# Optimization experiments

Hardware: AMD Instinct MI355X
Metric: run time of the kernel (lower is better)

The kernel has to match this reference:

```python
import jax, jax.numpy as jnp
import numpy as np

D_MODEL = 768
H = 12
D_K = D_MODEL // H
B = 2
S = 2048
NEG = -1e9


def setup_inputs() -> dict:
    key = jax.random.key(0)
    ks = jax.random.split(key, 12)
    scale = 1.0 / np.sqrt(D_MODEL)
    inp = {
        "q": jax.random.normal(ks[0], (B, S, D_MODEL), jnp.float32),
        "k": jax.random.normal(ks[1], (B, S, D_MODEL), jnp.float32),
        "v": jax.random.normal(ks[2], (B, S, D_MODEL), jnp.float32),
        "mask": jax.random.randint(ks[3], (B, 1, S, S), 0, 2, jnp.int32),
        "Wq": jax.random.normal(ks[4], (D_MODEL, D_MODEL), jnp.float32) * scale,
        "bq": jnp.zeros((D_MODEL,), jnp.float32),
        "Wk": jax.random.normal(ks[5], (D_MODEL, D_MODEL), jnp.float32) * scale,
        "bk": jnp.zeros((D_MODEL,), jnp.float32),
        "Wv": jax.random.normal(ks[6], (D_MODEL, D_MODEL), jnp.float32) * scale,
        "bv": jnp.zeros((D_MODEL,), jnp.float32),
        "Wo": jax.random.normal(ks[7], (D_MODEL, D_MODEL), jnp.float32) * scale,
        "bo": jnp.zeros((D_MODEL,), jnp.float32),
    }
    return inp


def _split_heads(x):
    # [B, S, D] -> [B, H, S, D_K]
    b, s, _ = x.shape
    return x.reshape(b, s, H, D_K).transpose(0, 2, 1, 3)


def reference(q, k, v, mask, Wq, bq, Wk, bk, Wv, bv, Wo, bo):
    # torch Linear: x @ W.T + b
    query = _split_heads(q @ Wq.T + bq)
    key_ = _split_heads(k @ Wk.T + bk)
    value = _split_heads(v @ Wv.T + bv)

    scores = jnp.einsum("bhqd,bhkd->bhqk", query, key_) / np.sqrt(D_K)
    scores = jnp.where(mask == 0, NEG, scores)
    attn = jax.nn.softmax(scores, axis=-1)  # dropout p=0.0 -> identity

    x = jnp.einsum("bhqk,bhkd->bhqd", attn, value)
    x = x.transpose(0, 2, 1, 3).reshape(q.shape[0], -1, D_MODEL)
    return x @ Wo.T + bo
```

## Files before the change

### kernel.cpp

```cpp
#include <hip/hip_runtime.h>
#include <math.h>

#define DMODEL 768
#define NHEAD 12
#define DKDIM 64
#define BB 2
#define SS 2048
#define MROWS (BB * SS)
#define WELEM (DMODEL * DMODEL)

typedef unsigned short bf16_t;
typedef __attribute__((ext_vector_type(8))) short s8;
typedef __attribute__((ext_vector_type(4))) float f4;

#define MFMA(a, b, c) __builtin_amdgcn_mfma_f32_16x16x32_bf16((a), (b), (c), 0, 0, 0)

__device__ __forceinline__ bf16_t f2bf(float f) {
    unsigned u = __float_as_uint(f);
    u += 0x7fffu + ((u >> 16) & 1u);
    return (bf16_t)(u >> 16);
}
__device__ __forceinline__ unsigned pack2(float a, float b) {
    return (unsigned)f2bf(a) | ((unsigned)f2bf(b) << 16);
}
__device__ __forceinline__ s8 ldfrag(const bf16_t* p) {
    union { uint4 u; s8 s; } x;
    x.u = *(const uint4*)p;
    return x.s;
}

__device__ __forceinline__ void ld_stage(const bf16_t* p, uint4& u0, uint4& u1) {
    u0 = *(const uint4*)p;
    u1 = *(const uint4*)(p + 8);
}
__device__ __forceinline__ void ld_stage(const float* p, uint4& u0, uint4& u1) {
    const float4 f0 = *(const float4*)p;
    const float4 f1 = *(const float4*)(p + 4);
    const float4 f2 = *(const float4*)(p + 8);
    const float4 f3 = *(const float4*)(p + 12);
    u0.x = pack2(f0.x, f0.y); u0.y = pack2(f0.z, f0.w);
    u0.z = pack2(f1.x, f1.y); u0.w = pack2(f1.z, f1.w);
    u1.x = pack2(f2.x, f2.y); u1.y = pack2(f2.z, f2.w);
    u1.z = pack2(f3.x, f3.y); u1.w = pack2(f3.z, f3.w);
}

__global__ void cvt_weights(const float* __restrict__ W0, const float* __restrict__ W1,
                            const float* __restrict__ W2, const float* __restrict__ W3,
                            bf16_t* __restrict__ dst)
{
    const float* src = (blockIdx.y == 0) ? W0 : (blockIdx.y == 1) ? W1
                     : (blockIdx.y == 2) ? W2 : W3;
    bf16_t* d = dst + (size_t)blockIdx.y * WELEM;
    const int i = (blockIdx.x * 256 + threadIdx.x) * 4;
    const float4 v = *(const float4*)(src + i);
    ushort4 h;
    h.x = f2bf(v.x); h.y = f2bf(v.y); h.z = f2bf(v.z); h.w = f2bf(v.w);
    *(ushort4*)(d + i) = h;
}

template<typename TA, typename TO>
__global__ __launch_bounds__(256) void gemm_tiled(
    const TA* __restrict__ A0, const TA* __restrict__ A1, const TA* __restrict__ A2,
    const bf16_t* __restrict__ W0, const bf16_t* __restrict__ W1, const bf16_t* __restrict__ W2,
    const float* __restrict__ bias0, const float* __restrict__ bias1, const float* __restrict__ bias2,
    TO* __restrict__ C0, TO* __restrict__ C1, TO* __restrict__ C2)
{
    __shared__ uint4 As4[128 * 4];
    __shared__ uint4 Bs4[128 * 4];

    const int z = blockIdx.z;
    const TA*     A    = (z == 0) ? A0 : (z == 1) ? A1 : A2;
    const bf16_t* W    = (z == 0) ? W0 : (z == 1) ? W1 : W2;
    const float*  bias = (z == 0) ? bias0 : (z == 1) ? bias1 : bias2;
    TO*           C    = (z == 0) ? C0 : (z == 1) ? C1 : C2;

    const int tid  = threadIdx.x;
    const int lane = tid & 63;
    const int w    = tid >> 6;
    const int wm   = w & 1;
    const int wn   = w >> 1;
    const int l15  = lane & 15;
    const int quad = lane >> 4;
    const int m0   = blockIdx.y * 128;
    const int n0   = blockIdx.x * 128;

    const int srow  = tid >> 1;
    const int shalf = tid & 1;
    const int sw    = srow & 3;

    const TA*     aptr = A + (size_t)(m0 + srow) * DMODEL + shalf * 16;
    const bf16_t* wptr = W + (size_t)(n0 + srow) * DMODEL + shalf * 16;

    f4 acc[4][4];
    #pragma unroll
    for (int i = 0; i < 4; i++)
        #pragma unroll
        for (int j = 0; j < 4; j++)
            acc[i][j] = (f4){0.f, 0.f, 0.f, 0.f};

    for (int k0 = 0; k0 < DMODEL; k0 += 32) {
        uint4 au0, au1, bu0, bu1;
        ld_stage(aptr + k0, au0, au1);
        ld_stage(wptr + k0, bu0, bu1);
        __syncthreads();
        As4[srow * 4 + ((shalf * 2 + 0) ^ sw)] = au0;
        As4[srow * 4 + ((shalf * 2 + 1) ^ sw)] = au1;
        Bs4[srow * 4 + ((shalf * 2 + 0) ^ sw)] = bu0;
        Bs4[srow * 4 + ((shalf * 2 + 1) ^ sw)] = bu1;
        __syncthreads();

        s8 af[4], bf[4];
        #pragma unroll
        for (int t = 0; t < 4; t++) {
            const int ar = wm * 64 + t * 16 + l15;
            const int br = wn * 64 + t * 16 + l15;
            union { uint4 u; s8 s; } xa, xb;
            xa.u = As4[ar * 4 + (quad ^ (ar & 3))];
            xb.u = Bs4[br * 4 + (quad ^ (br & 3))];
            af[t] = xa.s;
            bf[t] = xb.s;
        }
        #pragma unroll
        for (int mt = 0; mt < 4; mt++)
            #pragma unroll
            for (int nt = 0; nt < 4; nt++)
                acc[mt][nt] = MFMA(af[mt], bf[nt], acc[mt][nt]);
    }

    #pragma unroll
    for (int mt = 0; mt < 4; mt++) {
        #pragma unroll
        for (int nt = 0; nt < 4; nt++) {
            const int col = n0 + wn * 64 + nt * 16 + l15;
            const float bb = bias[col];
            #pragma unroll
            for (int reg = 0; reg < 4; reg++) {
                const int row = m0 + wm * 64 + mt * 16 + quad * 4 + reg;
                const float val = acc[mt][nt][reg] + bb;
                TO* dst = C + (size_t)row * DMODEL + col;
                if constexpr (sizeof(TO) == 2) *dst = f2bf(val);
                else                           *dst = val;
            }
        }
    }
}

__global__ __launch_bounds__(256) void attn_mfma(
    const bf16_t* __restrict__ Q, const bf16_t* __restrict__ K,
    const bf16_t* __restrict__ V, const int* __restrict__ mask,
    bf16_t* __restrict__ O)
{
    __shared__ unsigned Vs[64][36];
    __shared__ unsigned Ps[4][16][36];

    const int tid  = threadIdx.x;
    const int lane = tid & 63;
    const int w    = tid >> 6;
    const int l15  = lane & 15;
    const int quad = lane >> 4;
    const int q0   = blockIdx.x * 64;
    const int h    = blockIdx.y;
    const int b    = blockIdx.z;
    const size_t base = ((size_t)b * SS) * DMODEL + (size_t)h * DKDIM;

    const bf16_t* qrow = Q + base + (size_t)(q0 + w * 16 + l15) * DMODEL + quad * 8;
    const s8 qf0 = ldfrag(qrow);
    const s8 qf1 = ldfrag(qrow + 32);

    f4 oacc[4];
    float m_run[4], l_run[4];
    #pragma unroll
    for (int i = 0; i < 4; i++) {
        oacc[i] = (f4){0.f, 0.f, 0.f, 0.f};
        m_run[i] = -3.0e30f; l_run[i] = 0.0f;
    }

    const int kp  = tid & 31;
    const int oct = tid >> 5;

    const int* mrow = mask + (size_t)b * SS * SS + (size_t)(q0 + w * 16 + quad * 4) * SS;

    for (int k0 = 0; k0 < SS; k0 += 64) {
        const bf16_t* vrow = V + base + (size_t)(k0 + 2 * kp) * DMODEL + oct * 8;
        const uint4 va = *(const uint4*)vrow;
        const uint4 vb = *(const uint4*)(vrow + DMODEL);
        __syncthreads();
        {
            const unsigned short* pa = (const unsigned short*)&va;
            const unsigned short* pb = (const unsigned short*)&vb;
            #pragma unroll
            for (int i = 0; i < 8; i++)
                Vs[oct * 8 + i][kp] = (unsigned)pa[i] | ((unsigned)pb[i] << 16);
        }

        f4 sacc[4];
        #pragma unroll
        for (int nt = 0; nt < 4; nt++) {
            const bf16_t* krow = K + base + (size_t)(k0 + nt * 16 + l15) * DMODEL + quad * 8;
            f4 zz = {0.f, 0.f, 0.f, 0.f};
            zz = MFMA(qf0, ldfrag(krow), zz);
            zz = MFMA(qf1, ldfrag(krow + 32), zz);
            sacc[nt] = zz;
        }

        float p[4][4];
        #pragma unroll
        for (int reg = 0; reg < 4; reg++) {
            float sv[4];
            #pragma unroll
            for (int nt = 0; nt < 4; nt++) {
                const int mk = mrow[(size_t)reg * SS + k0 + nt * 16 + l15];
                sv[nt] = mk ? sacc[nt][reg] * 0.125f : -1.0e9f;
            }
            float mx = fmaxf(fmaxf(sv[0], sv[1]), fmaxf(sv[2], sv[3]));
            mx = fmaxf(mx, __shfl_xor(mx, 1, 16));
            mx = fmaxf(mx, __shfl_xor(mx, 2, 16));
            mx = fmaxf(mx, __shfl_xor(mx, 4, 16));
            mx = fmaxf(mx, __shfl_xor(mx, 8, 16));

            const float m_new = fmaxf(m_run[reg], mx);
            const float alpha = __expf(m_run[reg] - m_new);
            float rs = 0.f;
            #pragma unroll
            for (int nt = 0; nt < 4; nt++) {
                p[reg][nt] = __expf(sv[nt] - m_new);
                rs += p[reg][nt];
            }
            rs += __shfl_xor(rs, 1, 16);
            rs += __shfl_xor(rs, 2, 16);
            rs += __shfl_xor(rs, 4, 16);
            rs += __shfl_xor(rs, 8, 16);

            l_run[reg] = l_run[reg] * alpha + rs;
            m_run[reg] = m_new;
            #pragma unroll
            for (int dt = 0; dt < 4; dt++) oacc[dt][reg] *= alpha;
        }

        #pragma unroll
        for (int reg = 0; reg < 4; reg++) {
            #pragma unroll
            for (int nt = 0; nt < 4; nt++) {
                const float mine  = p[reg][nt];
                const float other = __shfl_xor(mine, 1, 16);
                if ((lane & 1) == 0)
                    Ps[w][quad * 4 + reg][nt * 8 + (l15 >> 1)] = pack2(mine, other);
            }
        }
        __syncthreads();

        #pragma unroll
        for (int kt = 0; kt < 2; kt++) {
            union { uint4 u; s8 s; } pf;
            pf.u = *(const uint4*)&Ps[w][l15][kt * 16 + quad * 4];
            #pragma unroll
            for (int dt = 0; dt < 4; dt++) {
                union { uint4 u; s8 s; } vf;
                vf.u = *(const uint4*)&Vs[dt * 16 + l15][kt * 16 + quad * 4];
                oacc[dt] = MFMA(pf.s, vf.s, oacc[dt]);
            }
        }
    }

    #pragma unroll
    for (int reg = 0; reg < 4; reg++) {
        const float inv = 1.0f / l_run[reg];
        #pragma unroll
        for (int dt = 0; dt < 4; dt++) {
            O[base + (size_t)(q0 + w * 16 + quad * 4 + reg) * DMODEL + dt * 16 + l15] =
                f2bf(oacc[dt][reg] * inv);
        }
    }
}

extern "C" void kernel_launch(void* const* d_in, const int* in_sizes, int n_in,
                              void* d_out, int out_size, void* d_ws, size_t ws_size,
                              hipStream_t stream)
{
    const float* q    = (const float*)d_in[0];
    const float* k    = (const float*)d_in[1];
    const float* v    = (const float*)d_in[2];
    const int*   mask = (const int*)  d_in[3];
    const float* Wq   = (const float*)d_in[4];
    const float* bq   = (const float*)d_in[5];
    const float* Wk   = (const float*)d_in[6];
    const float* bk   = (const float*)d_in[7];
    const float* Wv   = (const float*)d_in[8];
    const float* bv   = (const float*)d_in[9];
    const float* Wo   = (const float*)d_in[10];
    const float* bo   = (const float*)d_in[11];
    float* out = (float*)d_out;

    bf16_t* wsb = (bf16_t*)d_ws;
    const size_t plane = (size_t)MROWS * DMODEL;
    bf16_t* Qp  = wsb;
    bf16_t* Kp  = wsb + plane;
    bf16_t* Vp  = wsb + 2 * plane;
    bf16_t* Ctx = wsb + 3 * plane;
    bf16_t* Wqb = wsb + 4 * plane;
    bf16_t* Wkb = Wqb + WELEM;
    bf16_t* Wvb = Wkb + WELEM;
    bf16_t* Wob = Wvb + WELEM;

    cvt_weights<<<dim3(WELEM / 1024, 4), 256, 0, stream>>>(Wq, Wk, Wv, Wo, Wqb);

    gemm_tiled<float, bf16_t><<<dim3(DMODEL / 128, MROWS / 128, 3), 256, 0, stream>>>(
        q, k, v, Wqb, Wkb, Wvb, bq, bk, bv, Qp, Kp, Vp);

    attn_mfma<<<dim3(SS / 64, NHEAD, BB), 256, 0, stream>>>(Qp, Kp, Vp, mask, Ctx);

    gemm_tiled<bf16_t, float><<<dim3(DMODEL / 128, MROWS / 128, 1), 256, 0, stream>>>(
        Ctx, Ctx, Ctx, Wob, Wob, Wob, bo, bo, bo, out, out, out);
}
```

Measured before the change: 342.9 us.

## Bit-pack mask, split attention over keys, prefetch V, fold softmax scale into Q

Adds a pre-pass that packs the int32 mask into 64-bit ballot words, so the attention kernel reads one word per row per key tile instead of many int loads that are re-read for every head. The attention kernel is split into two key halves to double the grid, with a separate combine kernel that merges the partial outputs using the saved max and sum. V loads are register-prefetched one tile ahead, and the 1/sqrt(dk) scale is moved into the Q projection epilogue. The split adds fp32 partial-output traffic and an extra launch, and the mask pre-pass still reads the full 32 MB mask once.

```diff
diff --git a/kernel.cpp b/kernel.cpp
--- a/kernel.cpp
+++ b/kernel.cpp
@@ -8,6 +8,10 @@
 #define SS 2048
 #define MROWS (BB * SS)
 #define WELEM (DMODEL * DMODEL)
+#define NSPLIT 2
+#define KCHUNK (SS / NSPLIT)
+#define AROWS (BB * NHEAD * SS)
+#define MWORDS (SS / 64)
 
 typedef unsigned short bf16_t;
 typedef __attribute__((ext_vector_type(8))) short s8;
@@ -58,12 +62,22 @@
     *(ushort4*)(d + i) = h;
 }
 
+__global__ __launch_bounds__(256) void mask_to_bits(
+    const int* __restrict__ mask, unsigned long long* __restrict__ mbits)
+{
+    const size_t gid = (size_t)blockIdx.x * 256 + threadIdx.x;
+    const int m = mask[gid];
+    const unsigned long long bal = __ballot(m != 0);
+    if ((threadIdx.x & 63) == 0) mbits[gid >> 6] = bal;
+}
+
 template<typename TA, typename TO>
 __global__ __launch_bounds__(256) void gemm_tiled(
     const TA* __restrict__ A0, const TA* __restrict__ A1, const TA* __restrict__ A2,
     const bf16_t* __restrict__ W0, const bf16_t* __restrict__ W1, const bf16_t* __restrict__ W2,
     const float* __restrict__ bias0, const float* __restrict__ bias1, const float* __restrict__ bias2,
-    TO* __restrict__ C0, TO* __restrict__ C1, TO* __restrict__ C2)
+    TO* __restrict__ C0, TO* __restrict__ C1, TO* __restrict__ C2,
+    float sc0, float sc1, float sc2)
 {
     __shared__ uint4 As4[128 * 4];
     __shared__ uint4 Bs4[128 * 4];
@@ -73,6 +87,7 @@
     const bf16_t* W    = (z == 0) ? W0 : (z == 1) ? W1 : W2;
     const float*  bias = (z == 0) ? bias0 : (z == 1) ? bias1 : bias2;
     TO*           C    = (z == 0) ? C0 : (z == 1) ? C1 : C2;
+    const float   sc   = (z == 0) ? sc0 : (z == 1) ? sc1 : sc2;
 
     const int tid  = threadIdx.x;
     const int lane = tid & 63;
@@ -136,7 +151,7 @@
             #pragma unroll
             for (int reg = 0; reg < 4; reg++) {
                 const int row = m0 + wm * 64 + mt * 16 + quad * 4 + reg;
-                const float val = acc[mt][nt][reg] + bb;
+                const float val = (acc[mt][nt][reg] + bb) * sc;
                 TO* dst = C + (size_t)row * DMODEL + col;
                 if constexpr (sizeof(TO) == 2) *dst = f2bf(val);
                 else                           *dst = val;
@@ -145,10 +160,10 @@
     }
 }
 
-__global__ __launch_bounds__(256) void attn_mfma(
+__global__ __launch_bounds__(256, 6) void attn_mfma(
     const bf16_t* __restrict__ Q, const bf16_t* __restrict__ K,
-    const bf16_t* __restrict__ V, const int* __restrict__ mask,
-    bf16_t* __restrict__ O)
+    const bf16_t* __restrict__ V, const unsigned long long* __restrict__ mbits,
+    float* __restrict__ Opart, float2* __restrict__ Ml)
 {
     __shared__ unsigned Vs[64][36];
     __shared__ unsigned Ps[4][16][36];
@@ -160,7 +175,10 @@
     const int quad = lane >> 4;
     const int q0   = blockIdx.x * 64;
     const int h    = blockIdx.y;
-    const int b    = blockIdx.z;
+    const int zz   = blockIdx.z;
+    const int b     = zz >> 1;
+    const int split = zz & 1;
+    const int ks    = split * KCHUNK;
     const size_t base = ((size_t)b * SS) * DMODEL + (size_t)h * DKDIM;
 
     const bf16_t* qrow = Q + base + (size_t)(q0 + w * 16 + l15) * DMODEL + quad * 8;
@@ -177,13 +195,15 @@
 
     const int kp  = tid & 31;
     const int oct = tid >> 5;
-
-    const int* mrow = mask + (size_t)b * SS * SS + (size_t)(q0 + w * 16 + quad * 4) * SS;
-
-    for (int k0 = 0; k0 < SS; k0 += 64) {
-        const bf16_t* vrow = V + base + (size_t)(k0 + 2 * kp) * DMODEL + oct * 8;
-        const uint4 va = *(const uint4*)vrow;
-        const uint4 vb = *(const uint4*)(vrow + DMODEL);
+    const bf16_t* vbase = V + base + (size_t)(2 * kp) * DMODEL + oct * 8;
+
+    const unsigned long long* mbase =
+        mbits + ((size_t)b * SS + (q0 + w * 16 + quad * 4)) * MWORDS;
+
+    uint4 va = *(const uint4*)(vbase + (size_t)ks * DMODEL);
+    uint4 vb = *(const uint4*)(vbase + (size_t)ks * DMODEL + DMODEL);
+
+    for (int k0 = ks; k0 < ks + KCHUNK; k0 += 64) {
         __syncthreads();
         {
             const unsigned short* pa = (const unsigned short*)&va;
@@ -192,26 +212,36 @@
             for (int i = 0; i < 8; i++)
                 Vs[oct * 8 + i][kp] = (unsigned)pa[i] | ((unsigned)pb[i] << 16);
         }
+        if (k0 + 64 < ks + KCHUNK) {
+            va = *(const uint4*)(vbase + (size_t)(k0 + 64) * DMODEL);
+            vb = *(const uint4*)(vbase + (size_t)(k0 + 64) * DMODEL + DMODEL);
+        }
+        unsigned long long mw[4];
+        #pragma unroll
+        for (int reg = 0; reg < 4; reg++)
+            mw[reg] = mbase[(size_t)reg * MWORDS + (k0 >> 6)];
 
         f4 sacc[4];
         #pragma unroll
         for (int nt = 0; nt < 4; nt++) {
             const bf16_t* krow = K + base + (size_t)(k0 + nt * 16 + l15) * DMODEL + quad * 8;
-            f4 zz = {0.f, 0.f, 0.f, 0.f};
-            zz = MFMA(qf0, ldfrag(krow), zz);
-            zz = MFMA(qf1, ldfrag(krow + 32), zz);
-            sacc[nt] = zz;
+            f4 zz2 = {0.f, 0.f, 0.f, 0.f};
+            zz2 = MFMA(qf0, ldfrag(krow), zz2);
+            zz2 = MFMA(qf1, ldfrag(krow + 32), zz2);
+            sacc[nt] = zz2;
         }
 
         float p[4][4];
         #pragma unroll
         for (int reg = 0; reg < 4; reg++) {
+            const unsigned mlo = ((unsigned)mw[reg]) >> l15;
+            const unsigned mhi = ((unsigned)(mw[reg] >> 32)) >> l15;
             float sv[4];
-            #pragma unroll
-            for (int nt = 0; nt < 4; nt++) {
-                const int mk = mrow[(size_t)reg * SS + k0 + nt * 16 + l15];
-                sv[nt] = mk ? sacc[nt][reg] * 0.125f : -1.0e9f;
-            }
+            sv[0] = (mlo & 1u)       ? sacc[0][reg] : -1.0e9f;
+            sv[1] = (mlo & 0x10000u) ? sacc[1][reg] : -1.0e9f;
+            sv[2] = (mhi & 1u)       ? sacc[2][reg] : -1.0e9f;
+            sv[3] = (mhi & 0x10000u) ? sacc[3][reg] : -1.0e9f;
+
             float mx = fmaxf(fmaxf(sv[0], sv[1]), fmaxf(sv[2], sv[3]));
             mx = fmaxf(mx, __shfl_xor(mx, 1, 16));
             mx = fmaxf(mx, __shfl_xor(mx, 2, 16));
@@ -262,15 +292,51 @@
         }
     }
 
+    const int rid0 = (b * NHEAD + h) * SS + q0 + w * 16 + quad * 4;
     #pragma unroll
     for (int reg = 0; reg < 4; reg++) {
-        const float inv = 1.0f / l_run[reg];
-        #pragma unroll
-        for (int dt = 0; dt < 4; dt++) {
-            O[base + (size_t)(q0 + w * 16 + quad * 4 + reg) * DMODEL + dt * 16 + l15] =
-                f2bf(oacc[dt][reg] * inv);
-        }
-    }
+        float* dst = Opart + ((size_t)split * AROWS + rid0 + reg) * DKDIM;
+        #pragma unroll
+        for (int dt = 0; dt < 4; dt++)
+            dst[dt * 16 + l15] = oacc[dt][reg];
+        if (l15 == 0)
+            Ml[(size_t)split * AROWS + rid0 + reg] = make_float2(m_run[reg], l_run[reg]);
+    }
+}
+
+__global__ __launch_bounds__(256) void attn_combine(
+    const float* __restrict__ Opart, const float2* __restrict__ Ml,
+    bf16_t* __restrict__ Ctx)
+{
+    const int gid   = blockIdx.x * 256 + threadIdx.x;
+    const int rid   = gid >> 2;
+    const int dpart = (gid & 3) * 16;
+
+    const float2 ml0 = Ml[rid];
+    const float2 ml1 = Ml[AROWS + rid];
+    const float m   = fmaxf(ml0.x, ml1.x);
+    const float w0  = __expf(ml0.x - m);
+    const float w1  = __expf(ml1.x - m);
+    const float inv = 1.0f / (ml0.y * w0 + ml1.y * w1);
+
+    const float* o0 = Opart + (size_t)rid * DKDIM + dpart;
+    const float* o1 = o0 + (size_t)AROWS * DKDIM;
+
+    const int q  = rid & (SS - 1);
+    const int bh = rid >> 11;
+    const int hh = bh % NHEAD;
+    const int bb = bh / NHEAD;
+    bf16_t* dst = Ctx + ((size_t)bb * SS + q) * DMODEL + hh * DKDIM + dpart;
+
+    unsigned out[8];
+    #pragma unroll
+    for (int i = 0; i < 8; i++) {
+        const float a = (o0[2 * i]     * w0 + o1[2 * i]     * w1) * inv;
+        const float c = (o0[2 * i + 1] * w0 + o1[2 * i + 1] * w1) * inv;
+        out[i] = pack2(a, c);
+    }
+    *(uint4*)dst       = *(const uint4*)&out[0];
+    *(uint4*)(dst + 8) = *(const uint4*)&out[4];
 }
 
 extern "C" void kernel_launch(void* const* d_in, const int* in_sizes, int n_in,
@@ -301,14 +367,21 @@
     bf16_t* Wkb = Wqb + WELEM;
     bf16_t* Wvb = Wkb + WELEM;
     bf16_t* Wob = Wvb + WELEM;
+    float*  Opart = (float*)(Wob + WELEM);
+    float2* Ml    = (float2*)(Opart + (size_t)NSPLIT * AROWS * DKDIM);
+    unsigned long long* mbits = (unsigned long long*)(Ml + (size_t)NSPLIT * AROWS);
 
     cvt_weights<<<dim3(WELEM / 1024, 4), 256, 0, stream>>>(Wq, Wk, Wv, Wo, Wqb);
+    mask_to_bits<<<dim3((BB * SS * SS) / 256), 256, 0, stream>>>(mask, mbits);
 
     gemm_tiled<float, bf16_t><<<dim3(DMODEL / 128, MROWS / 128, 3), 256, 0, stream>>>(
-        q, k, v, Wqb, Wkb, Wvb, bq, bk, bv, Qp, Kp, Vp);
-
-    attn_mfma<<<dim3(SS / 64, NHEAD, BB), 256, 0, stream>>>(Qp, Kp, Vp, mask, Ctx);
+        q, k, v, Wqb, Wkb, Wvb, bq, bk, bv, Qp, Kp, Vp, 0.125f, 1.0f, 1.0f);
+
+    attn_mfma<<<dim3(SS / 64, NHEAD, BB * NSPLIT), 256, 0, stream>>>(
+        Qp, Kp, Vp, mbits, Opart, Ml);
+
+    attn_combine<<<dim3((AROWS * 4) / 256), 256, 0, stream>>>(Opart, Ml, Ctx);
 
     gemm_tiled<bf16_t, float><<<dim3(DMODEL / 128, MROWS / 128, 1), 256, 0, stream>>>(
-        Ctx, Ctx, Ctx, Wob, Wob, Wob, bo, bo, bo, out, out, out);
-}
+        Ctx, Ctx, Ctx, Wob, Wob, Wob, bo, bo, bo, out, out, out, 1.0f, 1.0f, 1.0f);
+}
```

After: 397.6 us. 15.9% more time.
